# Kernel optimization log

Measured on AMD Instinct MI355X. Metric: run time of the kernel, lower is better.

Reference implementation:

```python
import jax, jax.numpy as jnp
import numpy as np

B, H, LQ, LV, D = 32, 8, 256, 1024, 512


def setup_inputs() -> dict:
    key = jax.random.key(0)
    ks = jax.random.split(key, 10)
    sc = 0.02
    return {
        "queries": jax.random.normal(ks[0], (B, H, LQ, D), jnp.float32),
        "keys": jax.random.normal(ks[1], (B, LV, D), jnp.float32),
        "values": jax.random.normal(ks[2], (B, LV, D), jnp.float32),
        "W_q": sc * jax.random.normal(ks[3], (D, D), jnp.float32),
        "W_k": sc * jax.random.normal(ks[4], (D, D), jnp.float32),
        "W_v": sc * jax.random.normal(ks[5], (D, D), jnp.float32),
        "W_o": sc * jax.random.normal(ks[6], (D, D), jnp.float32),
        "W_len": sc * jax.random.normal(ks[7], (LQ, LV), jnp.float32),
        "b_len": sc * jax.random.normal(ks[8], (LQ,), jnp.float32),
        "valid_lens": jax.random.randint(ks[9], (B,), 0, LQ).astype(jnp.int32),
    }


def _multi_len_att(x, W_len, b_len):
    # x: [B, LV, D]; torch does permute(0,2,1) then Linear(LV->LQ) then
    # permute back; the identical linear is repeated per head (broadcast).
    # result per head: [B, LQ, D]
    return jnp.einsum('bld,ql->bqd', x, W_len) + b_len[None, :, None]


def reference(queries, keys, values, W_q, W_k, W_v, W_o, W_len, b_len, valid_lens):
    # queries: [B, H, LQ, D] -> W_q -> merge batch/head
    q = jnp.einsum('bhqd,ed->bhqe', queries, W_q).reshape(B * H, LQ, D)
    # keys/values: length-projection (shared across heads), then W_k/W_v
    k1 = jnp.einsum('bqd,ed->bqe', _multi_len_att(keys, W_len, b_len), W_k)   # [B, LQ, D]
    v1 = jnp.einsum('bqd,ed->bqe', _multi_len_att(values, W_len, b_len), W_v)  # [B, LQ, D]
    k = jnp.broadcast_to(k1[:, None], (B, H, LQ, D)).reshape(B * H, LQ, D)
    v = jnp.broadcast_to(v1[:, None], (B, H, LQ, D)).reshape(B * H, LQ, D)
    # scaled dot-product attention with valid-length masking
    scores = jnp.einsum('nqd,nkd->nqk', q, k) / jnp.sqrt(jnp.float32(D))  # [B*H, LQ, LQ]
    vl = jnp.repeat(valid_lens, H)                                        # [B*H]
    mask = jnp.arange(LQ)[None, None, :] < vl[:, None, None]
    scores = jnp.where(mask, scores, jnp.float32(-1e6))
    attn = jax.nn.softmax(scores, axis=-1)
    out = jnp.einsum('nqk,nkd->nqd', attn, v).reshape(B, H, LQ, D)
    return jnp.einsum('bhqd,ed->bhqe', out, W_o)
```

## Files before the change

kernel.cpp:

```cpp
#include <hip/hip_runtime.h>
#include <math.h>

#define Bc  32
#define Hc  8
#define LQc 256
#define LVc 1024
#define Dc  512

#define VMCNT0 asm volatile("s_waitcnt vmcnt(0)" ::: "memory")

typedef short bf16x8 __attribute__((ext_vector_type(8)));
typedef float f32x4  __attribute__((ext_vector_type(4)));

__device__ __forceinline__ unsigned short f2bf(float x) {
    unsigned u = __builtin_bit_cast(unsigned, x);
    u = (u + 0x7fffu + ((u >> 16) & 1u)) >> 16;
    return (unsigned short)u;
}

__device__ __forceinline__ bf16x8 pack8(float4 a, float4 b) {
    bf16x8 r;
    r[0] = (short)f2bf(a.x); r[1] = (short)f2bf(a.y);
    r[2] = (short)f2bf(a.z); r[3] = (short)f2bf(a.w);
    r[4] = (short)f2bf(b.x); r[5] = (short)f2bf(b.y);
    r[6] = (short)f2bf(b.z); r[7] = (short)f2bf(b.w);
    return r;
}

__device__ __forceinline__ void gload16(const ushort* g, ushort* l) {
    __builtin_amdgcn_global_load_lds(
        (const __attribute__((address_space(1))) unsigned*)g,
        (__attribute__((address_space(3))) unsigned*)l, 16, 0, 0);
}

__global__ __launch_bounds__(256) void prep_w(const float* __restrict__ Wq,
                                              const float* __restrict__ Wk,
                                              const float* __restrict__ Wv,
                                              const float* __restrict__ Wo,
                                              const float* __restrict__ Wl,
                                              ushort* __restrict__ wqT,
                                              ushort* __restrict__ wkT,
                                              ushort* __restrict__ wvT,
                                              ushort* __restrict__ woBf,
                                              ushort* __restrict__ wlBf) {
    const int z = blockIdx.z;
    if (z < 3) {
        __shared__ float t[32][33];
        const float* in = (z == 0) ? Wq : (z == 1) ? Wk : Wv;
        ushort* out = (z == 0) ? wqT : (z == 1) ? wkT : wvT;
        const int l0 = blockIdx.x * 32, d0 = blockIdx.y * 32;
        const int r = threadIdx.x >> 5, c = threadIdx.x & 31;
#pragma unroll
        for (int i = 0; i < 4; i++)
            t[r + 8 * i][c] = in[(size_t)(l0 + r + 8 * i) * 512 + d0 + c];
        __syncthreads();
#pragma unroll
        for (int i = 0; i < 4; i++)
            out[(size_t)(d0 + r + 8 * i) * 512 + l0 + c] = f2bf(t[c][r + 8 * i]);
    } else {
        const float* in = (z == 3) ? Wo : Wl;
        ushort* out = (z == 3) ? woBf : wlBf;
        const int i = (blockIdx.y * 16 + blockIdx.x) * 256 + threadIdx.x;
        float4 v = ((const float4*)in)[i];
        ushort4 o;
        o.x = f2bf(v.x); o.y = f2bf(v.y); o.z = f2bf(v.z); o.w = f2bf(v.w);
        ((ushort4*)out)[i] = o;
    }
}

__global__ __launch_bounds__(256) void transpose_kv(const float* __restrict__ keys,
                                                    const float* __restrict__ vals,
                                                    ushort* __restrict__ outK) {
    __shared__ float t[32][33];
    const int z = blockIdx.z;
    const float* in = ((z < 32) ? keys : vals) + (size_t)(z & 31) * LVc * Dc;
    ushort* out = outK + (size_t)z * LVc * Dc;
    const int l0 = blockIdx.x * 32, d0 = blockIdx.y * 32;
    const int r = threadIdx.x >> 5, c = threadIdx.x & 31;
#pragma unroll
    for (int i = 0; i < 4; i++)
        t[r + 8 * i][c] = in[(size_t)(l0 + r + 8 * i) * Dc + d0 + c];
    __syncthreads();
#pragma unroll
    for (int i = 0; i < 4; i++)
        out[(size_t)(d0 + r + 8 * i) * LVc + l0 + c] = f2bf(t[c][r + 8 * i]);
}

template <int STORE, bool BIAS, int SWIZ>
__global__ __launch_bounds__(256) void gemm_bt(const ushort* __restrict__ A,
                                               const ushort* __restrict__ B,
                                               void* __restrict__ Cv,
                                               const float* __restrict__ bias,
                                               int M, int N, int K, float alpha,
                                               long sA, long sB, long sC,
                                               int byPerXcd) {
    __shared__ ushort As[128 * 32];
    __shared__ ushort Bs[128 * 32];
    const int z = blockIdx.z;
    A += (size_t)z * sA;
    B += (size_t)z * sB;
    float*  Cf = (float*)Cv  + (size_t)z * sC;
    ushort* Ch = (ushort*)Cv + (size_t)z * sC;

    int bm, bn;
    if constexpr (SWIZ) {
        const int bid = blockIdx.x;
        const int xcd = bid & 7, slot = bid >> 3;
        bm = (xcd * byPerXcd + (slot >> 2)) * 128;
        bn = (slot & 3) * 128;
    } else {
        bm = blockIdx.y * 128;
        bn = blockIdx.x * 128;
    }
    const int tid = threadIdx.x;
    const int wave = tid >> 6, l = tid & 63;
    const int wm = (wave >> 1) * 64, wn = (wave & 1) * 64;
    const int l15 = l & 15, lh = l >> 4;

    f32x4 acc[4][4];
#pragma unroll
    for (int m = 0; m < 4; m++)
#pragma unroll
        for (int n = 0; n < 4; n++) acc[m][n] = (f32x4){0.f, 0.f, 0.f, 0.f};

    const int srow = tid >> 2, scol = (tid & 3) * 8;
    ushort* ldsA = As + (wave * 16) * 32;
    ushort* ldsB = Bs + (wave * 16) * 32;
    const ushort* gA = A + (size_t)(bm + srow) * K + scol;
    const ushort* gB = B + (size_t)(bn + srow) * K + scol;

    for (int k0 = 0; k0 < K; k0 += 32) {
        gload16(gA + k0, ldsA);
        gload16(gA + k0 + (size_t)64 * K, ldsA + 64 * 32);
        gload16(gB + k0, ldsB);
        gload16(gB + k0 + (size_t)64 * K, ldsB + 64 * 32);
        VMCNT0;
        __syncthreads();
        bf16x8 af[4], bfr[4];
#pragma unroll
        for (int m = 0; m < 4; m++)
            af[m] = *(const bf16x8*)&As[(wm + m * 16 + l15) * 32 + lh * 8];
#pragma unroll
        for (int n = 0; n < 4; n++)
            bfr[n] = *(const bf16x8*)&Bs[(wn + n * 16 + l15) * 32 + lh * 8];
#pragma unroll
        for (int m = 0; m < 4; m++)
#pragma unroll
            for (int n = 0; n < 4; n++)
                acc[m][n] = __builtin_amdgcn_mfma_f32_16x16x32_bf16(
                    af[m], bfr[n], acc[m][n], 0, 0, 0);
        __syncthreads();
    }

    if constexpr (STORE == 2) {
#pragma unroll
        for (int m = 0; m < 4; m++) {
            const int row0 = bm + wm + m * 16 + lh * 4;
            const int bb = row0 >> 8, q = row0 & 255;
            float bv[4] = {0.f, 0.f, 0.f, 0.f};
            if constexpr (BIAS) {
#pragma unroll
                for (int r = 0; r < 4; r++) bv[r] = bias[q + r];
            }
#pragma unroll
            for (int n = 0; n < 4; n++) {
                const int col = bn + wn + n * 16 + l15;
                ushort4 o;
                o.x = f2bf(acc[m][n][0] * alpha + bv[0]);
                o.y = f2bf(acc[m][n][1] * alpha + bv[1]);
                o.z = f2bf(acc[m][n][2] * alpha + bv[2]);
                o.w = f2bf(acc[m][n][3] * alpha + bv[3]);
                *(ushort4*)&Ch[(size_t)bb * N * 256 + (size_t)col * 256 + q] = o;
            }
        }
    } else if constexpr (STORE == 1) {
#pragma unroll
        for (int m = 0; m < 4; m++)
#pragma unroll
            for (int r = 0; r < 4; r++) {
                const int row = bm + wm + m * 16 + lh * 4 + r;
                const float bv = BIAS ? bias[row & 255] : 0.f;
#pragma unroll
                for (int n = 0; n < 4; n++) {
                    const int col = bn + wn + n * 16 + l15;
                    Ch[(size_t)row * N + col] = f2bf(acc[m][n][r] * alpha + bv);
                }
            }
    } else {
#pragma unroll
        for (int m = 0; m < 4; m++)
#pragma unroll
            for (int r = 0; r < 4; r++) {
                const int row = bm + wm + m * 16 + lh * 4 + r;
                const float bv = BIAS ? bias[row & 255] : 0.f;
#pragma unroll
                for (int n = 0; n < 4; n++) {
                    const int col = bn + wn + n * 16 + l15;
                    Cf[(size_t)row * N + col] = acc[m][n][r] * alpha + bv;
                }
            }
    }
}

__global__ __launch_bounds__(256, 2) void attn_mfma(const float* __restrict__ qf,
                                                    const ushort* __restrict__ k2,
                                                    const ushort* __restrict__ v2T,
                                                    const int* __restrict__ vlen,
                                                    float* __restrict__ aout) {
    __shared__ __align__(16) ushort pool[40960];
    ushort* Ps = pool;

    const int bid = blockIdx.x;
    const int xcd = bid & 7, pos = bid >> 3;
    const int b = xcd * 4 + (pos >> 4);
    const int inner = pos & 15;
    const int h = inner >> 1, qh = inner & 1;
    const int n = b * 8 + h;
    const int q0 = qh * 128;

    const int tid = threadIdx.x, wave = tid >> 6, l = tid & 63;
    const int l15 = l & 15, lh = l >> 4;
    const int vl = vlen[b];

    const float*  qbase = qf  + ((size_t)n * LQc + q0) * Dc;
    const ushort* kbase = k2  + (size_t)b * LQc * Dc;
    const ushort* vbase = v2T + (size_t)b * LQc * Dc;

    f32x4 sacc[2][16];
#pragma unroll
    for (int m = 0; m < 2; m++)
#pragma unroll
        for (int fn = 0; fn < 16; fn++) sacc[m][fn] = (f32x4){0.f, 0.f, 0.f, 0.f};

    auto STAGE_K = [&](int bi, int k0) {
        ushort* k_ = pool + bi * 8192;
#pragma unroll
        for (int j = 0; j < 4; j++)
            gload16(kbase + (size_t)((j * 4 + wave) * 16 + l15) * Dc + k0 + lh * 8,
                    k_ + (j * 4 + wave) * 512);
    };

    STAGE_K(0, 0);
    VMCNT0;
    __syncthreads();
    for (int t = 0; t < 16; ++t) {
        const int k0 = t * 32;
        if (t < 15) STAGE_K((t + 1) & 1, k0 + 32);
        bf16x8 aq[2];
#pragma unroll
        for (int m2 = 0; m2 < 2; ++m2) {
            const float* fb = qbase + (size_t)(wave * 32 + m2 * 16 + l15) * Dc + k0 + lh * 8;
            float4 x0 = *(const float4*)fb;
            float4 x1 = *(const float4*)(fb + 4);
            aq[m2] = pack8(x0, x1);
        }
        const ushort* k_ = pool + (t & 1) * 8192;
#pragma unroll
        for (int fn = 0; fn < 16; fn++) {
            bf16x8 bk = *(const bf16x8*)&k_[fn * 512 + lh * 128 + l15 * 8];
            sacc[0][fn] = __builtin_amdgcn_mfma_f32_16x16x32_bf16(aq[0], bk, sacc[0][fn], 0, 0, 0);
            sacc[1][fn] = __builtin_amdgcn_mfma_f32_16x16x32_bf16(aq[1], bk, sacc[1][fn], 0, 0, 0);
        }
        VMCNT0;
        __syncthreads();
    }

    auto STAGE_V = [&](int bi, int it) {
        const int d0 = (it >> 3) * 128, l0 = (it & 7) * 32;
        ushort* v_ = pool + 32768 + bi * 4096;
        gload16(vbase + (size_t)(d0 + wave * 16 + l15) * LQc + l0 + lh * 8,
                v_ + wave * 512);
        gload16(vbase + (size_t)(d0 + 64 + wave * 16 + l15) * LQc + l0 + lh * 8,
                v_ + (wave + 4) * 512);
    };
    STAGE_V(0, 0);

#pragma unroll
    for (int m = 0; m < 2; m++)
#pragma unroll
        for (int r = 0; r < 4; r++) {
            float v[16];
            float rmax = -3.4e38f;
#pragma unroll
            for (int fn = 0; fn < 16; fn++) {
                const int col = fn * 16 + l15;
                float s = sacc[m][fn][r];
                v[fn] = (col < vl) ? s : -1e6f;
                rmax = fmaxf(rmax, v[fn]);
            }
            rmax = fmaxf(rmax, __shfl_xor(rmax, 1));
            rmax = fmaxf(rmax, __shfl_xor(rmax, 2));
            rmax = fmaxf(rmax, __shfl_xor(rmax, 4));
            rmax = fmaxf(rmax, __shfl_xor(rmax, 8));
            float rsum = 0.f;
#pragma unroll
            for (int fn = 0; fn < 16; fn++) {
                v[fn] = __expf(v[fn] - rmax);
                rsum += v[fn];
            }
            rsum += __shfl_xor(rsum, 1);
            rsum += __shfl_xor(rsum, 2);
            rsum += __shfl_xor(rsum, 4);
            rsum += __shfl_xor(rsum, 8);
            const float rinv = 1.0f / rsum;
            const int base = (wave * 2 + m) * 4096 + (lh * 4 + r) * 8 + (l15 & 7);
            const int chi = (l15 >> 3) * 128;
#pragma unroll
            for (int fn = 0; fn < 16; fn++)
                Ps[base + fn * 256 + chi] = f2bf(v[fn] * rinv);
        }
    VMCNT0;
    __syncthreads();

    int it = 0;
    for (int d0 = 0; d0 < Dc; d0 += 128) {
        f32x4 o[8][2];
#pragma unroll
        for (int qf2 = 0; qf2 < 8; qf2++) {
            o[qf2][0] = (f32x4){0.f, 0.f, 0.f, 0.f};
            o[qf2][1] = (f32x4){0.f, 0.f, 0.f, 0.f};
        }
        for (int l0 = 0; l0 < LQc; l0 += 32, ++it) {
            if (it < 31) STAGE_V((it + 1) & 1, it + 1);
            const ushort* v_ = pool + 32768 + (it & 1) * 4096;
            bf16x8 vb[2];
            vb[0] = *(const bf16x8*)&v_[(2 * wave + 0) * 512 + lh * 128 + l15 * 8];
            vb[1] = *(const bf16x8*)&v_[(2 * wave + 1) * 512 + lh * 128 + l15 * 8];
            const int pcol = (l0 >> 3) + lh;
#pragma unroll
            for (int qf2 = 0; qf2 < 8; qf2++) {
                bf16x8 pa = *(const bf16x8*)&Ps[qf2 * 4096 + pcol * 128 + l15 * 8];
                o[qf2][0] = __builtin_amdgcn_mfma_f32_16x16x32_bf16(pa, vb[0], o[qf2][0], 0, 0, 0);
                o[qf2][1] = __builtin_amdgcn_mfma_f32_16x16x32_bf16(pa, vb[1], o[qf2][1], 0, 0, 0);
            }
            VMCNT0;
            __syncthreads();
        }
#pragma unroll
        for (int qf2 = 0; qf2 < 8; qf2++)
#pragma unroll
            for (int r = 0; r < 4; r++) {
                const int rowl = qf2 * 16 + lh * 4 + r;
#pragma unroll
                for (int df = 0; df < 2; df++) {
                    const int col = d0 + wave * 32 + df * 16 + l15;
                    aout[((size_t)n * LQc + q0 + rowl) * Dc + col] = o[qf2][df][r];
                }
            }
    }
}

extern "C" void kernel_launch(void* const* d_in, const int* in_sizes, int n_in,
                              void* d_out, int out_size, void* d_ws, size_t ws_size,
                              hipStream_t stream) {
    const float* queries    = (const float*)d_in[0];
    const float* keys       = (const float*)d_in[1];
    const float* values     = (const float*)d_in[2];
    const float* W_q        = (const float*)d_in[3];
    const float* W_k        = (const float*)d_in[4];
    const float* W_v        = (const float*)d_in[5];
    const float* W_o        = (const float*)d_in[6];
    const float* W_len      = (const float*)d_in[7];
    const float* b_len      = (const float*)d_in[8];
    const int*   valid_lens = (const int*)d_in[9];

    char* ws = (char*)d_ws;
    const size_t MB = 1024 * 1024;
    ushort* keysT   = (ushort*)(ws + 64 * MB);
    ushort* woBf = (ushort*)(ws + 128 * MB);
    ushort* wl   = woBf + 262144;
    ushort* wqT  = wl   + 262144;
    ushort* wkT  = wqT  + 262144;
    ushort* wvT  = wkT  + 262144;
    ushort* Eq   = wvT  + 262144;
    ushort* G    = Eq   + 262144;
    ushort* t1k  = G    + 262144;
    ushort* t1v  = t1k  + 4194304;
    ushort* k2   = t1v  + 4194304;
    ushort* v2T  = k2   + 4194304;

    const float alpha_q = 0.044194173824159216f;
    dim3 blk(256);

    prep_w<<<dim3(16, 16, 5), blk, 0, stream>>>(W_q, W_k, W_v, W_o, W_len,
                                                wqT, wkT, wvT, woBf, wl);
    gemm_bt<1, false, 0><<<dim3(4, 4, 1), blk, 0, stream>>>(
        wqT, wkT, Eq, nullptr, 512, 512, 512, 1.f, 0, 0, 0, 0);
    gemm_bt<1, false, 0><<<dim3(4, 4, 1), blk, 0, stream>>>(
        woBf, wvT, G, nullptr, 512, 512, 512, 1.f, 0, 0, 0, 0);

    transpose_kv<<<dim3(32, 16, 64), blk, 0, stream>>>(keys, values, keysT);

    gemm_bt<1, true, 0><<<dim3(4, 2, 64), blk, 0, stream>>>(
        wl, keysT, t1k, b_len, 256, 512, 1024, 1.f, 0, 524288, 131072, 0);

    gemm_bt<1, false, 1><<<dim3(256), blk, 0, stream>>>(
        t1k, Eq, k2, nullptr, 8192, 512, 512, alpha_q, 0, 0, 0, 8);
    gemm_bt<2, false, 1><<<dim3(256), blk, 0, stream>>>(
        t1v, G, v2T, nullptr, 8192, 512, 512, 1.f, 0, 0, 0, 8);

    attn_mfma<<<dim3(512), blk, 0, stream>>>(queries, k2, v2T, valid_lens,
                                             (float*)d_out);
}
```

Baseline: 219.4 us.

## Prefetch Q and V fragments into registers and relax vmcnt waits in attention

In the QK phase, the next tile's Q values are now loaded into registers alongside the K LDS staging. The loop is unrolled two-way and waits only with vmcnt(4), so the Q prefetch can stay in flight while MFMAs run. In the PV phase, V fragments are read from global memory straight into registers with double-buffering, which removes the V LDS staging and the per-iteration barriers and shrinks LDS to 64KB. The trade-offs are higher register pressure and reliance on correct vmcnt counting; the waits are tuned to the load count and could go wrong if the compiler reorders loads.

```diff
diff --git a/kernel.cpp b/kernel.cpp
--- a/kernel.cpp
+++ b/kernel.cpp
@@ -7,7 +7,7 @@
 #define LVc 1024
 #define Dc  512
 
-#define VMCNT0 asm volatile("s_waitcnt vmcnt(0)" ::: "memory")
+#define VMCNT(N) asm volatile("s_waitcnt vmcnt(" #N ")" ::: "memory")
 
 typedef short bf16x8 __attribute__((ext_vector_type(8)));
 typedef float f32x4  __attribute__((ext_vector_type(4)));
@@ -134,7 +134,7 @@
         gload16(gA + k0 + (size_t)64 * K, ldsA + 64 * 32);
         gload16(gB + k0, ldsB);
         gload16(gB + k0 + (size_t)64 * K, ldsB + 64 * 32);
-        VMCNT0;
+        VMCNT(0);
         __syncthreads();
         bf16x8 af[4], bfr[4];
 #pragma unroll
@@ -207,7 +207,7 @@
                                                     const ushort* __restrict__ v2T,
                                                     const int* __restrict__ vlen,
                                                     float* __restrict__ aout) {
-    __shared__ __align__(16) ushort pool[40960];
+    __shared__ __align__(16) ushort pool[32768];
     ushort* Ps = pool;
 
     const int bid = blockIdx.x;
@@ -239,41 +239,59 @@
             gload16(kbase + (size_t)((j * 4 + wave) * 16 + l15) * Dc + k0 + lh * 8,
                     k_ + (j * 4 + wave) * 512);
     };
-
-    STAGE_K(0, 0);
-    VMCNT0;
-    __syncthreads();
-    for (int t = 0; t < 16; ++t) {
-        const int k0 = t * 32;
-        if (t < 15) STAGE_K((t + 1) & 1, k0 + 32);
-        bf16x8 aq[2];
-#pragma unroll
-        for (int m2 = 0; m2 < 2; ++m2) {
-            const float* fb = qbase + (size_t)(wave * 32 + m2 * 16 + l15) * Dc + k0 + lh * 8;
-            float4 x0 = *(const float4*)fb;
-            float4 x1 = *(const float4*)(fb + 4);
-            aq[m2] = pack8(x0, x1);
-        }
-        const ushort* k_ = pool + (t & 1) * 8192;
+    auto QL = [&](int k0, float4& a0, float4& a1, float4& b0, float4& b1) {
+        const float* f0 = qbase + (size_t)(wave * 32 + l15) * Dc + k0 + lh * 8;
+        const float* f1 = qbase + (size_t)(wave * 32 + 16 + l15) * Dc + k0 + lh * 8;
+        a0 = *(const float4*)f0; a1 = *(const float4*)(f0 + 4);
+        b0 = *(const float4*)f1; b1 = *(const float4*)(f1 + 4);
+    };
+    auto MFMA_A = [&](int bufsel, bf16x8 aq0, bf16x8 aq1) {
+        const ushort* k_ = pool + bufsel * 8192;
 #pragma unroll
         for (int fn = 0; fn < 16; fn++) {
             bf16x8 bk = *(const bf16x8*)&k_[fn * 512 + lh * 128 + l15 * 8];
-            sacc[0][fn] = __builtin_amdgcn_mfma_f32_16x16x32_bf16(aq[0], bk, sacc[0][fn], 0, 0, 0);
-            sacc[1][fn] = __builtin_amdgcn_mfma_f32_16x16x32_bf16(aq[1], bk, sacc[1][fn], 0, 0, 0);
-        }
-        VMCNT0;
+            sacc[0][fn] = __builtin_amdgcn_mfma_f32_16x16x32_bf16(aq0, bk, sacc[0][fn], 0, 0, 0);
+            sacc[1][fn] = __builtin_amdgcn_mfma_f32_16x16x32_bf16(aq1, bk, sacc[1][fn], 0, 0, 0);
+        }
+    };
+
+    float4 pa0, pa1, pb0, pb1;
+    float4 ra0, ra1, rb0, rb1;
+    STAGE_K(0, 0);
+    __builtin_amdgcn_sched_barrier(0);
+    QL(0, pa0, pa1, pb0, pb1);
+    VMCNT(4);
+    __syncthreads();
+
+    for (int tp = 0; tp < 8; ++tp) {
+        const int te = tp * 2;
+        if (te < 15) {
+            STAGE_K((te + 1) & 1, (te + 1) * 32);
+            __builtin_amdgcn_sched_barrier(0);
+            QL((te + 1) * 32, ra0, ra1, rb0, rb1);
+        }
+        MFMA_A(te & 1, pack8(pa0, pa1), pack8(pb0, pb1));
+        VMCNT(4);
         __syncthreads();
-    }
-
-    auto STAGE_V = [&](int bi, int it) {
+
+        const int to = te + 1;
+        if (to < 15) {
+            STAGE_K((to + 1) & 1, (to + 1) * 32);
+            __builtin_amdgcn_sched_barrier(0);
+            QL((to + 1) * 32, pa0, pa1, pb0, pb1);
+        }
+        MFMA_A(to & 1, pack8(ra0, ra1), pack8(rb0, rb1));
+        VMCNT(4);
+        __syncthreads();
+    }
+
+    auto VL = [&](int it, bf16x8& v0, bf16x8& v1) {
         const int d0 = (it >> 3) * 128, l0 = (it & 7) * 32;
-        ushort* v_ = pool + 32768 + bi * 4096;
-        gload16(vbase + (size_t)(d0 + wave * 16 + l15) * LQc + l0 + lh * 8,
-                v_ + wave * 512);
-        gload16(vbase + (size_t)(d0 + 64 + wave * 16 + l15) * LQc + l0 + lh * 8,
-                v_ + (wave + 4) * 512);
+        v0 = *(const bf16x8*)(vbase + (size_t)(d0 + wave * 32 + l15) * LQc + l0 + lh * 8);
+        v1 = *(const bf16x8*)(vbase + (size_t)(d0 + wave * 32 + 16 + l15) * LQc + l0 + lh * 8);
     };
-    STAGE_V(0, 0);
+    bf16x8 vc0, vc1, vn0, vn1;
+    VL(0, vc0, vc1);
 
 #pragma unroll
     for (int m = 0; m < 2; m++)
@@ -309,32 +327,41 @@
             for (int fn = 0; fn < 16; fn++)
                 Ps[base + fn * 256 + chi] = f2bf(v[fn] * rinv);
         }
-    VMCNT0;
     __syncthreads();
 
     int it = 0;
-    for (int d0 = 0; d0 < Dc; d0 += 128) {
+    for (int d0i = 0; d0i < 4; ++d0i) {
+        const int d0 = d0i * 128;
         f32x4 o[8][2];
 #pragma unroll
         for (int qf2 = 0; qf2 < 8; qf2++) {
             o[qf2][0] = (f32x4){0.f, 0.f, 0.f, 0.f};
             o[qf2][1] = (f32x4){0.f, 0.f, 0.f, 0.f};
         }
-        for (int l0 = 0; l0 < LQc; l0 += 32, ++it) {
-            if (it < 31) STAGE_V((it + 1) & 1, it + 1);
-            const ushort* v_ = pool + 32768 + (it & 1) * 4096;
-            bf16x8 vb[2];
-            vb[0] = *(const bf16x8*)&v_[(2 * wave + 0) * 512 + lh * 128 + l15 * 8];
-            vb[1] = *(const bf16x8*)&v_[(2 * wave + 1) * 512 + lh * 128 + l15 * 8];
-            const int pcol = (l0 >> 3) + lh;
-#pragma unroll
-            for (int qf2 = 0; qf2 < 8; qf2++) {
-                bf16x8 pa = *(const bf16x8*)&Ps[qf2 * 4096 + pcol * 128 + l15 * 8];
-                o[qf2][0] = __builtin_amdgcn_mfma_f32_16x16x32_bf16(pa, vb[0], o[qf2][0], 0, 0, 0);
-                o[qf2][1] = __builtin_amdgcn_mfma_f32_16x16x32_bf16(pa, vb[1], o[qf2][1], 0, 0, 0);
-            }
-            VMCNT0;
-            __syncthreads();
+#pragma unroll
+        for (int l0p = 0; l0p < 4; ++l0p) {
+            if (it < 31) VL(it + 1, vn0, vn1);
+            {
+                const int pcol = (it & 7) * 4 + lh;
+#pragma unroll
+                for (int qf2 = 0; qf2 < 8; qf2++) {
+                    bf16x8 pa = *(const bf16x8*)&Ps[qf2 * 4096 + pcol * 128 + l15 * 8];
+                    o[qf2][0] = __builtin_amdgcn_mfma_f32_16x16x32_bf16(pa, vc0, o[qf2][0], 0, 0, 0);
+                    o[qf2][1] = __builtin_amdgcn_mfma_f32_16x16x32_bf16(pa, vc1, o[qf2][1], 0, 0, 0);
+                }
+            }
+            ++it;
+            if (it < 31) VL(it + 1, vc0, vc1);
+            {
+                const int pcol = (it & 7) * 4 + lh;
+#pragma unroll
+                for (int qf2 = 0; qf2 < 8; qf2++) {
+                    bf16x8 pa = *(const bf16x8*)&Ps[qf2 * 4096 + pcol * 128 + l15 * 8];
+                    o[qf2][0] = __builtin_amdgcn_mfma_f32_16x16x32_bf16(pa, vn0, o[qf2][0], 0, 0, 0);
+                    o[qf2][1] = __builtin_amdgcn_mfma_f32_16x16x32_bf16(pa, vn1, o[qf2][1], 0, 0, 0);
+                }
+            }
+            ++it;
         }
 #pragma unroll
         for (int qf2 = 0; qf2 < 8; qf2++)
```

Result: slower. 268.5 us (+22.4%).

## Fuse key/value transpose and bf16 conversion into length-projection GEMM

Applied to the files above, without the earlier changes.

Replaces the separate transpose_kv kernel and the following batched gemm_bt with a single lenproj_f32 kernel. It reads the fp32 keys/values directly, transposes them through shared memory, converts to bf16 on the fly and runs the MFMA GEMM against W_len with the bias added at the end. This removes writing and re-reading a 64 MB bf16 transposed intermediate plus one launch. In exchange it uses scalar transposed LDS stores, which may cause bank conflicts, and a simple unpipelined loop that waits on vmcnt(0) every step.

```diff
diff --git a/kernel.cpp b/kernel.cpp
--- a/kernel.cpp
+++ b/kernel.cpp
@@ -68,22 +68,95 @@
     }
 }
 
-__global__ __launch_bounds__(256) void transpose_kv(const float* __restrict__ keys,
-                                                    const float* __restrict__ vals,
-                                                    ushort* __restrict__ outK) {
-    __shared__ float t[32][33];
+__global__ __launch_bounds__(256) void lenproj_f32(const ushort* __restrict__ wl,
+                                                   const float* __restrict__ keys,
+                                                   const float* __restrict__ vals,
+                                                   const float* __restrict__ bias,
+                                                   ushort* __restrict__ t1k) {
+    __shared__ __align__(16) ushort Wls[4096];
+    __shared__ __align__(16) float  Xsf[128 * 36];
+
     const int z = blockIdx.z;
-    const float* in = ((z < 32) ? keys : vals) + (size_t)(z & 31) * LVc * Dc;
-    ushort* out = outK + (size_t)z * LVc * Dc;
-    const int l0 = blockIdx.x * 32, d0 = blockIdx.y * 32;
-    const int r = threadIdx.x >> 5, c = threadIdx.x & 31;
-#pragma unroll
-    for (int i = 0; i < 4; i++)
-        t[r + 8 * i][c] = in[(size_t)(l0 + r + 8 * i) * Dc + d0 + c];
-    __syncthreads();
-#pragma unroll
-    for (int i = 0; i < 4; i++)
-        out[(size_t)(d0 + r + 8 * i) * LVc + l0 + c] = f2bf(t[c][r + 8 * i]);
+    const float* X = ((z < 32) ? keys : vals) + (size_t)(z & 31) * LVc * Dc;
+    ushort* C = t1k + (size_t)z * LQc * Dc;
+
+    const int bm = blockIdx.y * 128;
+    const int bn = blockIdx.x * 128;
+    const int tid = threadIdx.x;
+    const int wave = tid >> 6, l = tid & 63;
+    const int wm = (wave >> 1) * 64, wn = (wave & 1) * 64;
+    const int l15 = l & 15, lh = l >> 4;
+
+    f32x4 acc[4][4];
+#pragma unroll
+    for (int m = 0; m < 4; m++)
+#pragma unroll
+        for (int n = 0; n < 4; n++) acc[m][n] = (f32x4){0.f, 0.f, 0.f, 0.f};
+
+    const int lrow = tid >> 3;
+    const int dcol = (tid & 7) * 16;
+
+    for (int l0 = 0; l0 < LVc; l0 += 32) {
+        gload16(wl + (size_t)(bm + wave * 16 + l15) * LVc + l0 + lh * 8,
+                Wls + wave * 512);
+        gload16(wl + (size_t)(bm + 64 + wave * 16 + l15) * LVc + l0 + lh * 8,
+                Wls + (wave + 4) * 512);
+        const float* xs = X + (size_t)(l0 + lrow) * Dc + bn + dcol;
+        float4 xv0 = ((const float4*)xs)[0];
+        float4 xv1 = ((const float4*)xs)[1];
+        float4 xv2 = ((const float4*)xs)[2];
+        float4 xv3 = ((const float4*)xs)[3];
+        Xsf[(dcol + 0)  * 36 + lrow] = xv0.x;
+        Xsf[(dcol + 1)  * 36 + lrow] = xv0.y;
+        Xsf[(dcol + 2)  * 36 + lrow] = xv0.z;
+        Xsf[(dcol + 3)  * 36 + lrow] = xv0.w;
+        Xsf[(dcol + 4)  * 36 + lrow] = xv1.x;
+        Xsf[(dcol + 5)  * 36 + lrow] = xv1.y;
+        Xsf[(dcol + 6)  * 36 + lrow] = xv1.z;
+        Xsf[(dcol + 7)  * 36 + lrow] = xv1.w;
+        Xsf[(dcol + 8)  * 36 + lrow] = xv2.x;
+        Xsf[(dcol + 9)  * 36 + lrow] = xv2.y;
+        Xsf[(dcol + 10) * 36 + lrow] = xv2.z;
+        Xsf[(dcol + 11) * 36 + lrow] = xv2.w;
+        Xsf[(dcol + 12) * 36 + lrow] = xv3.x;
+        Xsf[(dcol + 13) * 36 + lrow] = xv3.y;
+        Xsf[(dcol + 14) * 36 + lrow] = xv3.z;
+        Xsf[(dcol + 15) * 36 + lrow] = xv3.w;
+        VMCNT0;
+        __syncthreads();
+
+        bf16x8 af[4], bfr[4];
+#pragma unroll
+        for (int m = 0; m < 4; m++)
+            af[m] = *(const bf16x8*)&Wls[((wm >> 4) + m) * 512 + lh * 128 + l15 * 8];
+#pragma unroll
+        for (int n = 0; n < 4; n++) {
+            const float* fb = &Xsf[(wn + n * 16 + l15) * 36 + lh * 8];
+            float4 x0 = *(const float4*)fb;
+            float4 x1 = *(const float4*)(fb + 4);
+            bfr[n] = pack8(x0, x1);
+        }
+#pragma unroll
+        for (int m = 0; m < 4; m++)
+#pragma unroll
+            for (int n = 0; n < 4; n++)
+                acc[m][n] = __builtin_amdgcn_mfma_f32_16x16x32_bf16(
+                    af[m], bfr[n], acc[m][n], 0, 0, 0);
+        __syncthreads();
+    }
+
+#pragma unroll
+    for (int m = 0; m < 4; m++)
+#pragma unroll
+        for (int r = 0; r < 4; r++) {
+            const int row = bm + wm + m * 16 + lh * 4 + r;
+            const float bv = bias[row];
+#pragma unroll
+            for (int n = 0; n < 4; n++) {
+                const int col = bn + wn + n * 16 + l15;
+                C[(size_t)row * Dc + col] = f2bf(acc[m][n][r] + bv);
+            }
+        }
 }
 
 template <int STORE, bool BIAS, int SWIZ>
@@ -366,7 +439,6 @@
 
     char* ws = (char*)d_ws;
     const size_t MB = 1024 * 1024;
-    ushort* keysT   = (ushort*)(ws + 64 * MB);
     ushort* woBf = (ushort*)(ws + 128 * MB);
     ushort* wl   = woBf + 262144;
     ushort* wqT  = wl   + 262144;
@@ -389,10 +461,7 @@
     gemm_bt<1, false, 0><<<dim3(4, 4, 1), blk, 0, stream>>>(
         woBf, wvT, G, nullptr, 512, 512, 512, 1.f, 0, 0, 0, 0);
 
-    transpose_kv<<<dim3(32, 16, 64), blk, 0, stream>>>(keys, values, keysT);
-
-    gemm_bt<1, true, 0><<<dim3(4, 2, 64), blk, 0, stream>>>(
-        wl, keysT, t1k, b_len, 256, 512, 1024, 1.f, 0, 524288, 131072, 0);
+    lenproj_f32<<<dim3(4, 2, 64), blk, 0, stream>>>(wl, keys, values, b_len, t1k);
 
     gemm_bt<1, false, 1><<<dim3(256), blk, 0, stream>>>(
         t1k, Eq, k2, nullptr, 8192, 512, 512, alpha_q, 0, 0, 0, 8);
```

After: 220.5 us. No clear change (+0.5%).
